# Optimization experiments

Hardware: AMD Instinct MI355X
Metric: run time of the kernel (lower is better)

The kernel has to match this reference:

```python
import jax, jax.numpy as jnp
import numpy as np

T, B, IN, H = 256, 64, 1024, 1024


def setup_inputs() -> dict:
    key = jax.random.key(0)
    ks = jax.random.split(key, 16)
    s = 0.02
    def w(k, shape):
        return jax.random.normal(k, shape, jnp.float32) * s
    return {
        "x": jax.random.normal(ks[0], (T, B, IN), jnp.float32),
        # layer 0 (input IN -> H)
        "W0": w(ks[1], (3 * H, IN)), "b0": jnp.zeros((3 * H,), jnp.float32),
        "Ur0": w(ks[2], (H, H)), "Uz0": w(ks[3], (H, H)),
        "Un0": w(ks[4], (H, H)), "bn0": jnp.zeros((H,), jnp.float32),
        # layer 1 (input 2H -> H)
        "W1": w(ks[5], (3 * H, 2 * H)), "b1": jnp.zeros((3 * H,), jnp.float32),
        "Ur1": w(ks[6], (H, H)), "Uz1": w(ks[7], (H, H)),
        "Un1": w(ks[8], (H, H)), "bn1": jnp.zeros((H,), jnp.float32),
    }


def _gru_layer(x_proj, Ur, Uz, Un, bn):
    """Bidirectional GRU layer. x_proj: (T,B,3H). Returns (T,B,2H), h_fwd, h_bwd.
    use_transpose_U=False path: h-projections use U (i.e. h @ U.T, as nn.Linear)."""
    Bsz = x_proj.shape[1]
    h0 = jnp.zeros((Bsz, H), x_proj.dtype)

    def step(h, xp):
        r_x, z_x, n_x = jnp.split(xp, 3, axis=-1)
        r = jax.nn.sigmoid(r_x + h @ Ur.T)
        z = jax.nn.sigmoid(z_x + h @ Uz.T)
        n = jnp.tanh(n_x + r * (h @ Un.T + bn))
        h_new = (1.0 - z) * n + z * h
        return h_new, h_new

    h_fwd, fwd_out = jax.lax.scan(step, h0, x_proj)
    # backward direction: same cell (shared U), sequence reversed; scan
    # with reverse=True writes bwd_out[t] for the state after consuming t..T-1,
    # matching the torch loop `for t in range(T-1,-1,-1)`.
    h_bwd, bwd_out = jax.lax.scan(step, h0, x_proj, reverse=True)
    return jnp.concatenate([fwd_out, bwd_out], axis=-1), h_fwd, h_bwd


def reference(x, W0, b0, Ur0, Uz0, Un0, bn0, W1, b1, Ur1, Uz1, Un1, bn1):
    # layer 0: fused input projection once for both directions
    xp0 = jnp.einsum("tbi,gi->tbg", x, W0) + b0          # (T,B,3H)
    out0, hf0, hb0 = _gru_layer(xp0, Ur0, Uz0, Un0, bn0)  # (T,B,2H)
    # dropout = Identity (dropout=0.0)
    xp1 = jnp.einsum("tbi,gi->tbg", out0, W1) + b1        # (T,B,3H)
    out1, hf1, hb1 = _gru_layer(xp1, Ur1, Uz1, Un1, bn1)  # (T,B,2H)
    hidden = jnp.stack([hf0, hb0, hf1, hb1])              # (num_layers*2,B,H)
    return out1, hidden
```

## Files before the change

### kernel.cpp

```cpp
#include <hip/hip_runtime.h>
#include <stdint.h>

typedef short short8v __attribute__((ext_vector_type(8)));
typedef unsigned short u16x8 __attribute__((ext_vector_type(8)));
typedef float f32x4  __attribute__((ext_vector_type(4)));
typedef float f32x2  __attribute__((ext_vector_type(2)));
typedef unsigned long long u64;

__device__ inline uint16_t f2bf(float f){
  uint32_t u = __float_as_uint(f);
  uint32_t r = (u + 0x7fffu + ((u >> 16) & 1u)) >> 16;
  return (uint16_t)r;
}
__device__ inline float bf2f(uint16_t h){
  return __uint_as_float(((uint32_t)h) << 16);
}

__global__ void cvt_f32_bf16(const float* __restrict__ src, uint16_t* __restrict__ dst, int n4){
  int i = blockIdx.x * blockDim.x + threadIdx.x;
  int stride = gridDim.x * blockDim.x;
  for (; i < n4; i += stride){
    float4 v = ((const float4*)src)[i];
    uint64_t p = (uint64_t)f2bf(v.x)
               | ((uint64_t)f2bf(v.y) << 16)
               | ((uint64_t)f2bf(v.z) << 32)
               | ((uint64_t)f2bf(v.w) << 48);
    ((uint64_t*)dst)[i] = p;
  }
}

#define GL2LDS(g, l) __builtin_amdgcn_global_load_lds((const __attribute__((address_space(1))) unsigned int*)(g), (__attribute__((address_space(3))) unsigned int*)(l), 16, 0, 0)

__global__ __launch_bounds__(256) void gemm_bt_bias(
    const uint16_t* __restrict__ A, const uint16_t* __restrict__ Bw,
    const float* __restrict__ bias, uint16_t* __restrict__ C,
    int M, int N, int K)
{
  __shared__ uint16_t As[128 * 64];
  __shared__ uint16_t Bs[128 * 64];
  const int tid  = threadIdx.x;
  const int lane = tid & 63, wid = tid >> 6;
  const int n0 = blockIdx.x * 128, m0 = blockIdx.y * 128;
  const int wrow = (wid & 1) * 64, wcol = (wid >> 1) * 64;
  const int l15 = lane & 15, l4 = lane >> 4;
  const int srow = lane >> 3, scol = (lane & 7) * 8;
  const size_t Ks = (size_t)K;

  f32x4 acc[4][4] = {};

  for (int kt = 0; kt < K; kt += 64){
    __syncthreads();
    const uint16_t* gA = A  + (size_t)m0 * Ks + kt;
    const uint16_t* gB = Bw + (size_t)n0 * Ks + kt;
    #pragma unroll
    for (int i = 0; i < 4; ++i){
      int rb = wid * 32 + i * 8;
      GL2LDS(gA + (size_t)(rb + srow) * Ks + scol, &As[rb * 64]);
      GL2LDS(gB + (size_t)(rb + srow) * Ks + scol, &Bs[rb * 64]);
    }
    __syncthreads();
    #pragma unroll
    for (int kk = 0; kk < 2; ++kk){
      short8v a[4], b[4];
      int koff = kk * 32 + l4 * 8;
      #pragma unroll
      for (int mt = 0; mt < 4; ++mt) a[mt] = *(const short8v*)&As[(wrow + mt*16 + l15) * 64 + koff];
      #pragma unroll
      for (int nt = 0; nt < 4; ++nt) b[nt] = *(const short8v*)&Bs[(wcol + nt*16 + l15) * 64 + koff];
      #pragma unroll
      for (int mt = 0; mt < 4; ++mt)
        #pragma unroll
        for (int nt = 0; nt < 4; ++nt)
          acc[mt][nt] = __builtin_amdgcn_mfma_f32_16x16x32_bf16(a[mt], b[nt], acc[mt][nt], 0, 0, 0);
    }
  }
  #pragma unroll
  for (int mt = 0; mt < 4; ++mt)
    #pragma unroll
    for (int nt = 0; nt < 4; ++nt){
      int col = n0 + wcol + nt * 16 + l15;
      float bv = bias[col];
      int rbase = m0 + wrow + mt * 16 + l4 * 4;
      #pragma unroll
      for (int j = 0; j < 4; ++j)
        C[(size_t)(rbase + j) * (size_t)N + col] = f2bf(acc[mt][nt][j] + bv);
    }
}

__device__ inline int ridx(int w, int c, int m){
  return (w * 48 + c) * 72 + (m ^ ((c & 7) << 2));
}

#define HLOAD(dst, addr) \
  asm volatile("global_load_dwordx4 %0, %1, off sc0 sc1" : "=v"(dst) : "v"(addr) : "memory")
#define XPLOAD4(dst, addr) \
  asm volatile("global_load_dword %0, %1, off" : "=v"(dst) : "v"(addr) : "memory")
#define HSTORE4(addr, val) \
  asm volatile("global_store_dword %0, %1, off sc0 sc1" :: "v"(addr), "v"(val) : "memory")
#define OSTORE4(addr, val) \
  asm volatile("global_store_dword %0, %1, off nt" :: "v"(addr), "v"(val) : "memory")
#define OSTORE8(addr, val) \
  asm volatile("global_store_dwordx2 %0, %1, off nt" :: "v"(addr), "v"(val) : "memory")
#define WAITVM(n) do { asm volatile("s_waitcnt vmcnt(" #n ")" ::: "memory"); \
                       __builtin_amdgcn_sched_barrier(0); } while (0)

__global__ __launch_bounds__(256, 1) void gru_layer(
    const uint16_t* __restrict__ xp,
    const uint16_t* __restrict__ U,
    const float* __restrict__ bn,
    char* __restrict__ hring,
    uint16_t* __restrict__ out_bf,
    float* __restrict__ out_f32,
    float* __restrict__ hid)
{
  __shared__ float red[4 * 48 * 72];
  const int tid  = threadIdx.x;
  const int lane = tid & 63, wid = tid >> 6;
  const int bid  = blockIdx.x;
  const int dir  = bid >> 7;
  const int grp  = (bid >> 6) & 1;
  const int dg   = dir * 2 + grp;
  const int cb   = bid & 63;
  const int c0   = cb * 16;
  const int brow0 = grp * 32;
  const int l15 = lane & 15, l4 = lane >> 4;
  const int gm = tid >> 3;
  const int cp = (tid & 7) * 2;

  short8v bfr[3][8];
  #pragma unroll
  for (int g = 0; g < 3; ++g)
    #pragma unroll
    for (int k32 = 0; k32 < 8; ++k32){
      int row = g * 1024 + c0 + l15;
      int k   = wid * 256 + k32 * 32 + l4 * 8;
      bfr[g][k32] = *(const short8v*)&U[(size_t)row * 1024 + k];
    }

  float hold[2] = {0.f, 0.f};
  float bnv[2] = { bn[c0 + cp], bn[c0 + cp + 1] };

  const size_t hoff = (size_t)(wid * 16 + (l4 >> 1)) * 1024 + (size_t)(l4 & 1) * 16 + (size_t)l15 * 32;

  for (int s = 0; s < 256; ++s){
    const int t = dir ? (255 - s) : s;
    const size_t xb2 = ((size_t)t * 64 + brow0 + gm) * 3072 + c0 + cp;

    f32x4 acc[3][2] = {};
    unsigned pxr, pxz, pxn;
    if (s > 0){
      const char* hgbase = hring + ((size_t)((s & 31) * 4 + dg) * 64) * 1024;

      XPLOAD4(pxr, &xp[xb2]);
      XPLOAD4(pxz, &xp[xb2 + 1024]);
      XPLOAD4(pxn, &xp[xb2 + 2048]);
      short8v hc[8][2];
      #pragma unroll
      for (int c = 0; c < 8; ++c)
        #pragma unroll
        for (int mt = 0; mt < 2; ++mt)
          HLOAD(hc[c][mt], hgbase + hoff + (size_t)c * 2048 + (size_t)mt * 512);
      WAITVM(0);

      int spins = 0;
      for (;;){
        u16x8 mx = (u16x8)hc[0][0];
        #pragma unroll
        for (int c = 0; c < 8; ++c)
          #pragma unroll
          for (int mt = 0; mt < 2; ++mt)
            if (c | mt) mx = __builtin_elementwise_max(mx, (u16x8)hc[c][mt]);
        unsigned anybad = 0;
        #pragma unroll
        for (int i = 0; i < 8; ++i) anybad |= (unsigned)(mx[i] == (unsigned short)0xFFFFu);
        if (!__any((int)anybad)) break;
        __builtin_amdgcn_s_sleep(1);
        if (((++spins) & 255) == 0)
          __builtin_amdgcn_fence(__ATOMIC_ACQUIRE, "agent");
        #pragma unroll
        for (int c = 0; c < 8; ++c)
          #pragma unroll
          for (int mt = 0; mt < 2; ++mt)
            HLOAD(hc[c][mt], hgbase + hoff + (size_t)c * 2048 + (size_t)mt * 512);
        WAITVM(0);
      }

      #pragma unroll
      for (int kk = 0; kk < 8; ++kk)
        #pragma unroll
        for (int g = 0; g < 3; ++g)
          #pragma unroll
          for (int mt = 0; mt < 2; ++mt)
            acc[g][mt] = __builtin_amdgcn_mfma_f32_16x16x32_bf16(hc[kk][mt], bfr[g][kk], acc[g][mt], 0, 0, 0);
    } else {
      pxr = *(const unsigned*)&xp[xb2];
      pxz = *(const unsigned*)&xp[xb2 + 1024];
      pxn = *(const unsigned*)&xp[xb2 + 2048];
    }

    #pragma unroll
    for (int g = 0; g < 3; ++g)
      #pragma unroll
      for (int mt = 0; mt < 2; ++mt)
        *(f32x4*)&red[ridx(wid, g * 16 + l15, mt * 16 + l4 * 4)] = acc[g][mt];
    __syncthreads();

    float ra[2] = {}, za[2] = {}, na[2] = {};
    #pragma unroll
    for (int w = 0; w < 4; ++w)
      #pragma unroll
      for (int j = 0; j < 2; ++j){
        ra[j] += red[ridx(w,      cp + j, gm)];
        za[j] += red[ridx(w, 16 + cp + j, gm)];
        na[j] += red[ridx(w, 32 + cp + j, gm)];
      }
    __syncthreads();

    unsigned hv = 0;
    float hn[2];
    #pragma unroll
    for (int j = 0; j < 2; ++j){
      float xr = bf2f((uint16_t)(pxr >> (16 * j)));
      float xz = bf2f((uint16_t)(pxz >> (16 * j)));
      float xn = bf2f((uint16_t)(pxn >> (16 * j)));
      float r = 1.f / (1.f + __expf(-(xr + ra[j])));
      float z = 1.f / (1.f + __expf(-(xz + za[j])));
      float n = tanhf(xn + r * (na[j] + bnv[j]));
      hn[j] = (1.f - z) * n + z * hold[j];
      hold[j] = hn[j];
      hv |= ((unsigned)f2bf(hn[j])) << (16 * j);
    }

    {
      const size_t mybyte = (size_t)cb * 1024 + (size_t)gm * 32 + (size_t)cp * 2;
      char* hw = hring + ((size_t)(((s + 1) & 31) * 4 + dg) * 64) * 1024 + mybyte;
      HSTORE4(hw, hv);
      char* sw = hring + ((size_t)(((s + 17) & 31) * 4 + dg) * 64) * 1024 + mybyte;
      HSTORE4(sw, 0xFFFFFFFFu);
    }

    {
      size_t obase = ((size_t)t * 64 + brow0 + gm) * 2048 + (size_t)dir * 1024 + c0 + cp;
      if (out_bf) OSTORE4(&out_bf[obase], hv);
      else {
        f32x2 ov = { hn[0], hn[1] };
        OSTORE8(&out_f32[obase], ov);
      }
      if (s == 255){
        f32x2 hvv = { hn[0], hn[1] };
        *(f32x2*)&hid[((size_t)dir * 64 + brow0 + gm) * 1024 + c0 + cp] = hvv;
      }
    }
  }
}

extern "C" void kernel_launch(void* const* d_in, const int* in_sizes, int n_in,
                              void* d_out, int out_size, void* d_ws, size_t ws_size,
                              hipStream_t stream) {
  const float* x   = (const float*)d_in[0];
  const float* W0  = (const float*)d_in[1];
  const float* b0  = (const float*)d_in[2];
  const float* Ur0 = (const float*)d_in[3];
  const float* Uz0 = (const float*)d_in[4];
  const float* Un0 = (const float*)d_in[5];
  const float* bn0 = (const float*)d_in[6];
  const float* W1  = (const float*)d_in[7];
  const float* b1  = (const float*)d_in[8];
  const float* Ur1 = (const float*)d_in[9];
  const float* Uz1 = (const float*)d_in[10];
  const float* Un1 = (const float*)d_in[11];
  const float* bn1 = (const float*)d_in[12];
  float* out = (float*)d_out;

  const size_t RING = (size_t)8 * 1024 * 1024;
  char* base = (char*)d_ws;
  char*     hring = base;
  uint16_t* xb    = (uint16_t*)(base + RING);
  uint16_t* w0b   = xb    + (size_t)16384 * 1024;
  uint16_t* u0b   = w0b   + (size_t)3072 * 1024;
  uint16_t* w1b   = u0b   + (size_t)3072 * 1024;
  uint16_t* u1b   = w1b   + (size_t)3072 * 2048;
  uint16_t* xp    = u1b   + (size_t)3072 * 1024;
  uint16_t* out0b = xp    + (size_t)16384 * 3072;

  auto cvt = [&](const float* s, uint16_t* d, size_t n){
    int n4 = (int)(n / 4);
    int grid = (n4 + 255) / 256; if (grid > 2048) grid = 2048;
    hipLaunchKernelGGL(cvt_f32_bf16, dim3(grid), dim3(256), 0, stream, s, d, n4);
  };
  hipMemsetAsync(hring, 0xFF, RING, stream);

  cvt(x,   xb,  (size_t)16384 * 1024);
  cvt(W0,  w0b, (size_t)3072 * 1024);
  cvt(Ur0, u0b + 0 * (size_t)1024 * 1024, (size_t)1024 * 1024);
  cvt(Uz0, u0b + 1 * (size_t)1024 * 1024, (size_t)1024 * 1024);
  cvt(Un0, u0b + 2 * (size_t)1024 * 1024, (size_t)1024 * 1024);
  cvt(W1,  w1b, (size_t)3072 * 2048);
  cvt(Ur1, u1b + 0 * (size_t)1024 * 1024, (size_t)1024 * 1024);
  cvt(Uz1, u1b + 1 * (size_t)1024 * 1024, (size_t)1024 * 1024);
  cvt(Un1, u1b + 2 * (size_t)1024 * 1024, (size_t)1024 * 1024);

  hipLaunchKernelGGL(gemm_bt_bias, dim3(24, 128), dim3(256), 0, stream,
                     xb, w0b, b0, xp, 16384, 3072, 1024);
  hipLaunchKernelGGL(gru_layer, dim3(256), dim3(256), 0, stream,
                     xp, u0b, bn0, hring,
                     out0b, (float*)nullptr,
                     out + (size_t)33554432);
  hipMemsetAsync(hring, 0xFF, RING, stream);
  hipLaunchKernelGGL(gemm_bt_bias, dim3(24, 128), dim3(256), 0, stream,
                     out0b, w1b, b1, xp, 16384, 3072, 2048);
  hipLaunchKernelGGL(gru_layer, dim3(256), dim3(256), 0, stream,
                     xp, u1b, bn1, hring,
                     (uint16_t*)nullptr, out,
                     out + (size_t)33554432 + (size_t)2 * 64 * 1024);
}
```

Before: 2.267 ms.

## Split GRU recurrent matvec K across eight waves per block

The recurrent GRU kernel doubles its block size from 256 to 512 threads. Each of the eight waves now holds a 128-wide K slice of U (half the prior registers) and issues half as many h loads and MFMAs per step. The cross-wave LDS reduction grows to eight partials, and each thread finishes one output element instead of two. This is meant to shorten the per-step critical path of the serial recurrence, at the cost of narrower 16-bit global loads and stores, more reduction reads, and a wider barrier.

Result: faster. 2.116 ms (-6.7%).

```diff
diff --git a/kernel.cpp b/kernel.cpp
--- a/kernel.cpp
+++ b/kernel.cpp
@@ -4,7 +4,6 @@
 typedef short short8v __attribute__((ext_vector_type(8)));
 typedef unsigned short u16x8 __attribute__((ext_vector_type(8)));
 typedef float f32x4  __attribute__((ext_vector_type(4)));
-typedef float f32x2  __attribute__((ext_vector_type(2)));
 typedef unsigned long long u64;
 
 __device__ inline uint16_t f2bf(float f){
@@ -87,24 +86,24 @@
     }
 }
 
-__device__ inline int ridx(int w, int c, int m){
-  return (w * 48 + c) * 72 + (m ^ ((c & 7) << 2));
+__device__ inline int ridx8(int w, int c, int m){
+  return (w * 48 + c) * 40 + (m ^ ((c & 7) << 2));
 }
 
 #define HLOAD(dst, addr) \
   asm volatile("global_load_dwordx4 %0, %1, off sc0 sc1" : "=v"(dst) : "v"(addr) : "memory")
-#define XPLOAD4(dst, addr) \
-  asm volatile("global_load_dword %0, %1, off" : "=v"(dst) : "v"(addr) : "memory")
-#define HSTORE4(addr, val) \
-  asm volatile("global_store_dword %0, %1, off sc0 sc1" :: "v"(addr), "v"(val) : "memory")
+#define XPLOAD2(dst, addr) \
+  asm volatile("global_load_ushort %0, %1, off" : "=v"(dst) : "v"(addr) : "memory")
+#define HSTORE2(addr, val) \
+  asm volatile("global_store_short %0, %1, off sc0 sc1" :: "v"(addr), "v"(val) : "memory")
+#define OSTORE2(addr, val) \
+  asm volatile("global_store_short %0, %1, off nt" :: "v"(addr), "v"(val) : "memory")
 #define OSTORE4(addr, val) \
   asm volatile("global_store_dword %0, %1, off nt" :: "v"(addr), "v"(val) : "memory")
-#define OSTORE8(addr, val) \
-  asm volatile("global_store_dwordx2 %0, %1, off nt" :: "v"(addr), "v"(val) : "memory")
 #define WAITVM(n) do { asm volatile("s_waitcnt vmcnt(" #n ")" ::: "memory"); \
                        __builtin_amdgcn_sched_barrier(0); } while (0)
 
-__global__ __launch_bounds__(256, 1) void gru_layer(
+__global__ __launch_bounds__(512, 1) void gru_layer(
     const uint16_t* __restrict__ xp,
     const uint16_t* __restrict__ U,
     const float* __restrict__ bn,
@@ -113,7 +112,7 @@
     float* __restrict__ out_f32,
     float* __restrict__ hid)
 {
-  __shared__ float red[4 * 48 * 72];
+  __shared__ float red[8 * 48 * 40];
   const int tid  = threadIdx.x;
   const int lane = tid & 63, wid = tid >> 6;
   const int bid  = blockIdx.x;
@@ -124,52 +123,52 @@
   const int c0   = cb * 16;
   const int brow0 = grp * 32;
   const int l15 = lane & 15, l4 = lane >> 4;
-  const int gm = tid >> 3;
-  const int cp = (tid & 7) * 2;
-
-  short8v bfr[3][8];
+  const int gm = tid >> 4;
+  const int c16 = tid & 15;
+
+  short8v bfr[3][4];
   #pragma unroll
   for (int g = 0; g < 3; ++g)
     #pragma unroll
-    for (int k32 = 0; k32 < 8; ++k32){
+    for (int kk = 0; kk < 4; ++kk){
       int row = g * 1024 + c0 + l15;
-      int k   = wid * 256 + k32 * 32 + l4 * 8;
-      bfr[g][k32] = *(const short8v*)&U[(size_t)row * 1024 + k];
-    }
-
-  float hold[2] = {0.f, 0.f};
-  float bnv[2] = { bn[c0 + cp], bn[c0 + cp + 1] };
-
-  const size_t hoff = (size_t)(wid * 16 + (l4 >> 1)) * 1024 + (size_t)(l4 & 1) * 16 + (size_t)l15 * 32;
+      int k   = wid * 128 + kk * 32 + l4 * 8;
+      bfr[g][kk] = *(const short8v*)&U[(size_t)row * 1024 + k];
+    }
+
+  float hold = 0.f;
+  const float bnv = bn[c0 + c16];
+
+  const size_t hoff = (size_t)(wid * 8 + (l4 >> 1)) * 1024 + (size_t)(l4 & 1) * 16 + (size_t)l15 * 32;
 
   for (int s = 0; s < 256; ++s){
     const int t = dir ? (255 - s) : s;
-    const size_t xb2 = ((size_t)t * 64 + brow0 + gm) * 3072 + c0 + cp;
+    const size_t xb2 = ((size_t)t * 64 + brow0 + gm) * 3072 + c0 + c16;
 
     f32x4 acc[3][2] = {};
     unsigned pxr, pxz, pxn;
     if (s > 0){
       const char* hgbase = hring + ((size_t)((s & 31) * 4 + dg) * 64) * 1024;
 
-      XPLOAD4(pxr, &xp[xb2]);
-      XPLOAD4(pxz, &xp[xb2 + 1024]);
-      XPLOAD4(pxn, &xp[xb2 + 2048]);
-      short8v hc[8][2];
-      #pragma unroll
-      for (int c = 0; c < 8; ++c)
+      XPLOAD2(pxr, &xp[xb2]);
+      XPLOAD2(pxz, &xp[xb2 + 1024]);
+      XPLOAD2(pxn, &xp[xb2 + 2048]);
+      short8v hc[4][2];
+      #pragma unroll
+      for (int kk = 0; kk < 4; ++kk)
         #pragma unroll
         for (int mt = 0; mt < 2; ++mt)
-          HLOAD(hc[c][mt], hgbase + hoff + (size_t)c * 2048 + (size_t)mt * 512);
+          HLOAD(hc[kk][mt], hgbase + hoff + (size_t)kk * 2048 + (size_t)mt * 512);
       WAITVM(0);
 
       int spins = 0;
       for (;;){
         u16x8 mx = (u16x8)hc[0][0];
         #pragma unroll
-        for (int c = 0; c < 8; ++c)
+        for (int kk = 0; kk < 4; ++kk)
           #pragma unroll
           for (int mt = 0; mt < 2; ++mt)
-            if (c | mt) mx = __builtin_elementwise_max(mx, (u16x8)hc[c][mt]);
+            if (kk | mt) mx = __builtin_elementwise_max(mx, (u16x8)hc[kk][mt]);
         unsigned anybad = 0;
         #pragma unroll
         for (int i = 0; i < 8; ++i) anybad |= (unsigned)(mx[i] == (unsigned short)0xFFFFu);
@@ -178,78 +177,67 @@
         if (((++spins) & 255) == 0)
           __builtin_amdgcn_fence(__ATOMIC_ACQUIRE, "agent");
         #pragma unroll
-        for (int c = 0; c < 8; ++c)
+        for (int kk = 0; kk < 4; ++kk)
           #pragma unroll
           for (int mt = 0; mt < 2; ++mt)
-            HLOAD(hc[c][mt], hgbase + hoff + (size_t)c * 2048 + (size_t)mt * 512);
+            HLOAD(hc[kk][mt], hgbase + hoff + (size_t)kk * 2048 + (size_t)mt * 512);
         WAITVM(0);
       }
 
       #pragma unroll
-      for (int kk = 0; kk < 8; ++kk)
+      for (int kk = 0; kk < 4; ++kk)
         #pragma unroll
         for (int g = 0; g < 3; ++g)
           #pragma unroll
           for (int mt = 0; mt < 2; ++mt)
             acc[g][mt] = __builtin_amdgcn_mfma_f32_16x16x32_bf16(hc[kk][mt], bfr[g][kk], acc[g][mt], 0, 0, 0);
     } else {
-      pxr = *(const unsigned*)&xp[xb2];
-      pxz = *(const unsigned*)&xp[xb2 + 1024];
-      pxn = *(const unsigned*)&xp[xb2 + 2048];
+      pxr = xp[xb2];
+      pxz = xp[xb2 + 1024];
+      pxn = xp[xb2 + 2048];
     }
 
     #pragma unroll
     for (int g = 0; g < 3; ++g)
       #pragma unroll
       for (int mt = 0; mt < 2; ++mt)
-        *(f32x4*)&red[ridx(wid, g * 16 + l15, mt * 16 + l4 * 4)] = acc[g][mt];
+        *(f32x4*)&red[ridx8(wid, g * 16 + l15, mt * 16 + l4 * 4)] = acc[g][mt];
     __syncthreads();
 
-    float ra[2] = {}, za[2] = {}, na[2] = {};
-    #pragma unroll
-    for (int w = 0; w < 4; ++w)
-      #pragma unroll
-      for (int j = 0; j < 2; ++j){
-        ra[j] += red[ridx(w,      cp + j, gm)];
-        za[j] += red[ridx(w, 16 + cp + j, gm)];
-        na[j] += red[ridx(w, 32 + cp + j, gm)];
-      }
+    float ra = 0.f, za = 0.f, na = 0.f;
+    #pragma unroll
+    for (int w = 0; w < 8; ++w){
+      ra += red[ridx8(w,      c16, gm)];
+      za += red[ridx8(w, 16 + c16, gm)];
+      na += red[ridx8(w, 32 + c16, gm)];
+    }
     __syncthreads();
 
-    unsigned hv = 0;
-    float hn[2];
-    #pragma unroll
-    for (int j = 0; j < 2; ++j){
-      float xr = bf2f((uint16_t)(pxr >> (16 * j)));
-      float xz = bf2f((uint16_t)(pxz >> (16 * j)));
-      float xn = bf2f((uint16_t)(pxn >> (16 * j)));
-      float r = 1.f / (1.f + __expf(-(xr + ra[j])));
-      float z = 1.f / (1.f + __expf(-(xz + za[j])));
-      float n = tanhf(xn + r * (na[j] + bnv[j]));
-      hn[j] = (1.f - z) * n + z * hold[j];
-      hold[j] = hn[j];
-      hv |= ((unsigned)f2bf(hn[j])) << (16 * j);
-    }
+    WAITVM(0);
+    float xr = bf2f((uint16_t)pxr);
+    float xz = bf2f((uint16_t)pxz);
+    float xn = bf2f((uint16_t)pxn);
+    float r = 1.f / (1.f + __expf(-(xr + ra)));
+    float z = 1.f / (1.f + __expf(-(xz + za)));
+    float n = tanhf(xn + r * (na + bnv));
+    float hn = (1.f - z) * n + z * hold;
+    hold = hn;
+    unsigned hv = f2bf(hn);
 
     {
-      const size_t mybyte = (size_t)cb * 1024 + (size_t)gm * 32 + (size_t)cp * 2;
+      const size_t mybyte = (size_t)cb * 1024 + (size_t)gm * 32 + (size_t)c16 * 2;
       char* hw = hring + ((size_t)(((s + 1) & 31) * 4 + dg) * 64) * 1024 + mybyte;
-      HSTORE4(hw, hv);
+      HSTORE2(hw, hv);
       char* sw = hring + ((size_t)(((s + 17) & 31) * 4 + dg) * 64) * 1024 + mybyte;
-      HSTORE4(sw, 0xFFFFFFFFu);
+      HSTORE2(sw, 0xFFFFu);
     }
 
     {
-      size_t obase = ((size_t)t * 64 + brow0 + gm) * 2048 + (size_t)dir * 1024 + c0 + cp;
-      if (out_bf) OSTORE4(&out_bf[obase], hv);
-      else {
-        f32x2 ov = { hn[0], hn[1] };
-        OSTORE8(&out_f32[obase], ov);
-      }
-      if (s == 255){
-        f32x2 hvv = { hn[0], hn[1] };
-        *(f32x2*)&hid[((size_t)dir * 64 + brow0 + gm) * 1024 + c0 + cp] = hvv;
-      }
+      size_t obase = ((size_t)t * 64 + brow0 + gm) * 2048 + (size_t)dir * 1024 + c0 + c16;
+      if (out_bf) OSTORE2(&out_bf[obase], hv);
+      else        OSTORE4(&out_f32[obase], __float_as_uint(hn));
+      if (s == 255)
+        hid[((size_t)dir * 64 + brow0 + gm) * 1024 + c0 + c16] = hn;
     }
   }
 }
@@ -302,14 +290,14 @@
 
   hipLaunchKernelGGL(gemm_bt_bias, dim3(24, 128), dim3(256), 0, stream,
                      xb, w0b, b0, xp, 16384, 3072, 1024);
-  hipLaunchKernelGGL(gru_layer, dim3(256), dim3(256), 0, stream,
+  hipLaunchKernelGGL(gru_layer, dim3(256), dim3(512), 0, stream,
                      xp, u0b, bn0, hring,
                      out0b, (float*)nullptr,
                      out + (size_t)33554432);
   hipMemsetAsync(hring, 0xFF, RING, stream);
   hipLaunchKernelGGL(gemm_bt_bias, dim3(24, 128), dim3(256), 0, stream,
                      out0b, w1b, b1, xp, 16384, 3072, 2048);
-  hipLaunchKernelGGL(gru_layer, dim3(256), dim3(256), 0, stream,
+  hipLaunchKernelGGL(gru_layer, dim3(256), dim3(512), 0, stream,
                      xp, u1b, bn1, hring,
                      (uint16_t*)nullptr, out,
                      out + (size_t)33554432 + (size_t)2 * 64 * 1024);
```
